# Kernel tuning notes

Measured on AMD Instinct MI355X. Metric: run time of the kernel, lower is better.

The kernel has to match this reference:

```python
import jax, jax.numpy as jnp
import numpy as np

B, N, K, H, W = 8, 16, 128, 64, 64
POS_RATE = 0.002  # fraction of positive heatmap pixels


def setup_inputs() -> dict:
    key = jax.random.key(0)
    k1, k2, k3 = jax.random.split(key, 3)
    # scores in (0.01, 0.99) so log(s) and log(1-s) are finite
    all_scores = jax.random.uniform(k1, (B, K, N), dtype=jnp.float32) * 0.98 + 0.01
    gt_heatmap = (jax.random.uniform(k2, (B, N, H, W)) < POS_RATE).astype(jnp.float32)
    # guarantee at least one positive pixel per heatmap (original errors on empty nonzero)
    gt_heatmap = gt_heatmap.at[:, :, 0, 0].set(1.0)
    keypoints_list = jax.random.uniform(k3, (B, K, 2), dtype=jnp.float32) * H
    return {"all_scores": all_scores, "gt_heatmap": gt_heatmap, "keypoints_list": keypoints_list}


def reference(all_scores, gt_heatmap, keypoints_list):
    Bs, Ns, Hs, Ws = gt_heatmap.shape
    # pixel coordinates in (row, col) order, matching torch nonzero() output
    hh, ww = jnp.meshgrid(jnp.arange(Hs, dtype=jnp.float32),
                          jnp.arange(Ws, dtype=jnp.float32), indexing='ij')
    coords = jnp.stack([hh.ravel(), ww.ravel()], axis=-1)  # [HW, 2]

    # distance from every candidate keypoint to every pixel: [B, K, HW]
    diff = keypoints_list[:, :, None, :] - coords[None, None, :, :]
    dist = jnp.sqrt(jnp.sum(diff * diff, axis=-1))

    mask = gt_heatmap.reshape(Bs, Ns, -1) > 0  # [B, N, HW]
    # min distance to any ground-truth pixel of heatmap n: [B, N, K]
    dmin = jnp.min(jnp.where(mask[:, :, None, :], dist[:, None, :, :], jnp.inf), axis=-1)

    scores = jnp.transpose(all_scores, (0, 2, 1))  # [B, N, K]
    pos = dmin < 1.0
    dsafe = jnp.where(pos, dmin, 0.0)  # avoid inf/overflow in unused branch
    pos_loss = jnp.sum(jnp.where(pos, 10000.0 / (1.0 + jnp.exp(dsafe)) * jnp.log(scores), 0.0))
    neg_loss = jnp.sum(jnp.where(pos, 0.0, jnp.log(1.0 - scores)))
    neg_count = jnp.sum(~pos)

    loss = -pos_loss - jnp.where(neg_count > 0,
                                 10000.0 / neg_count.astype(jnp.float32) * neg_loss,
                                 0.0)
    return loss
```

## Files before the change

### kernel.cpp

```cpp
#include <hip/hip_runtime.h>

#define BB 8
#define NN 16
#define KK 128
#define HH 64
#define WW 64
#define HWPX (HH * WW)

__global__ __launch_bounds__(256) void kp_loss_partials(
    const float* __restrict__ all_scores,
    const float* __restrict__ gt_heatmap,
    const float* __restrict__ keypoints,
    float* __restrict__ partials)
{
    __shared__ float sh_r[HWPX];
    __shared__ float sh_c[HWPX];
    __shared__ int   sh_count;
    __shared__ float red0[256], red1[256], red2[256];

    const int blk = blockIdx.x;
    const int b   = blk / NN;
    const int n   = blk % NN;
    const int tid = threadIdx.x;

    if (tid == 0) sh_count = 0;
    __syncthreads();

    const float* hm = gt_heatmap + (size_t)blk * HWPX;
    for (int i = tid; i < HWPX; i += 256) {
        if (hm[i] > 0.0f) {
            int slot = atomicAdd(&sh_count, 1);
            sh_r[slot] = (float)(i >> 6);
            sh_c[slot] = (float)(i & (WW - 1));
        }
    }
    __syncthreads();
    const int cnt = sh_count;

    float pos_c = 0.0f, neg_c = 0.0f, ncnt = 0.0f;
    if (tid < KK) {
        const int k = tid;
        const float kr = keypoints[((size_t)b * KK + k) * 2 + 0];
        const float kc = keypoints[((size_t)b * KK + k) * 2 + 1];
        float dmin2 = INFINITY;
        for (int m = 0; m < cnt; ++m) {
            const float dr = kr - sh_r[m];
            const float dc = kc - sh_c[m];
            dmin2 = fminf(dmin2, dr * dr + dc * dc);
        }
        const float score = all_scores[((size_t)b * KK + k) * NN + n];
        if (dmin2 < 1.0f) {
            const float dmin = sqrtf(dmin2);
            pos_c = 10000.0f / (1.0f + __expf(dmin)) * __logf(score);
        } else {
            neg_c = __logf(1.0f - score);
            ncnt  = 1.0f;
        }
    }

    red0[tid] = pos_c; red1[tid] = neg_c; red2[tid] = ncnt;
    __syncthreads();
    for (int s = 128; s > 0; s >>= 1) {
        if (tid < s) {
            red0[tid] += red0[tid + s];
            red1[tid] += red1[tid + s];
            red2[tid] += red2[tid + s];
        }
        __syncthreads();
    }
    if (tid == 0) {
        partials[blk * 3 + 0] = red0[0];
        partials[blk * 3 + 1] = red1[0];
        partials[blk * 3 + 2] = red2[0];
    }
}

__global__ __launch_bounds__(128) void kp_loss_finalize(
    const float* __restrict__ partials, float* __restrict__ out)
{
    __shared__ float red0[128], red1[128], red2[128];
    const int tid = threadIdx.x;
    red0[tid] = partials[tid * 3 + 0];
    red1[tid] = partials[tid * 3 + 1];
    red2[tid] = partials[tid * 3 + 2];
    __syncthreads();
    for (int s = 64; s > 0; s >>= 1) {
        if (tid < s) {
            red0[tid] += red0[tid + s];
            red1[tid] += red1[tid + s];
            red2[tid] += red2[tid + s];
        }
        __syncthreads();
    }
    if (tid == 0) {
        const float pos_sum = red0[0];
        const float neg_sum = red1[0];
        const float cnt     = red2[0];
        float loss = -pos_sum;
        if (cnt > 0.0f) loss -= (10000.0f / cnt) * neg_sum;
        out[0] = loss;
    }
}

extern "C" void kernel_launch(void* const* d_in, const int* in_sizes, int n_in,
                              void* d_out, int out_size, void* d_ws, size_t ws_size,
                              hipStream_t stream) {
    const float* all_scores = (const float*)d_in[0];
    const float* gt_heatmap = (const float*)d_in[1];
    const float* keypoints  = (const float*)d_in[2];
    float* out = (float*)d_out;
    float* partials = (float*)d_ws;

    kp_loss_partials<<<BB * NN, 256, 0, stream>>>(all_scores, gt_heatmap, keypoints, partials);
    kp_loss_finalize<<<1, 128, 0, stream>>>(partials, out);
}
```

Measured before the change: 12.24 us.

## Fuse partial and final reduction into one cooperative kernel with grid sync

Merges the two kernels into a single cooperative launch that uses a grid-wide sync before block 0 reduces the per-block partials, removing the second launch. Blocks shrink from 256 to 128 threads so every thread handles a keypoint, heatmap loads are vectorised to float4, and the shared-memory tree reductions become wavefront shuffle reductions. A cooperative launch and grid barrier have their own overhead, and the atomic slot ordering now differs.

```diff
diff --git a/kernel.cpp b/kernel.cpp
--- a/kernel.cpp
+++ b/kernel.cpp
@@ -1,4 +1,7 @@
 #include <hip/hip_runtime.h>
+#include <hip/hip_cooperative_groups.h>
+
+namespace cg = cooperative_groups;
 
 #define BB 8
 #define NN 16
@@ -7,98 +10,93 @@
 #define WW 64
 #define HWPX (HH * WW)
 
-__global__ __launch_bounds__(256) void kp_loss_partials(
+__global__ __launch_bounds__(128) void kp_loss_fused(
     const float* __restrict__ all_scores,
     const float* __restrict__ gt_heatmap,
     const float* __restrict__ keypoints,
-    float* __restrict__ partials)
+    float* __restrict__ partials,
+    float* __restrict__ out)
 {
     __shared__ float sh_r[HWPX];
     __shared__ float sh_c[HWPX];
     __shared__ int   sh_count;
-    __shared__ float red0[256], red1[256], red2[256];
+    __shared__ float wred[2][3];
 
-    const int blk = blockIdx.x;
-    const int b   = blk / NN;
-    const int n   = blk % NN;
-    const int tid = threadIdx.x;
+    const int blk  = blockIdx.x;
+    const int b    = blk >> 4;
+    const int n    = blk & (NN - 1);
+    const int tid  = threadIdx.x;
+    const int lane = tid & 63;
+    const int wid  = tid >> 6;
 
     if (tid == 0) sh_count = 0;
     __syncthreads();
 
-    const float* hm = gt_heatmap + (size_t)blk * HWPX;
-    for (int i = tid; i < HWPX; i += 256) {
-        if (hm[i] > 0.0f) {
-            int slot = atomicAdd(&sh_count, 1);
-            sh_r[slot] = (float)(i >> 6);
-            sh_c[slot] = (float)(i & (WW - 1));
-        }
+    const float4* hm = (const float4*)(gt_heatmap + (size_t)blk * HWPX);
+    for (int i = tid; i < HWPX / 4; i += 128) {
+        const float4 v = hm[i];
+        const int base = i << 2;
+        const float row = (float)(base >> 6);
+        const float col = (float)(base & (WW - 1));
+        if (v.x > 0.0f) { int s = atomicAdd(&sh_count, 1); sh_r[s] = row; sh_c[s] = col; }
+        if (v.y > 0.0f) { int s = atomicAdd(&sh_count, 1); sh_r[s] = row; sh_c[s] = col + 1.0f; }
+        if (v.z > 0.0f) { int s = atomicAdd(&sh_count, 1); sh_r[s] = row; sh_c[s] = col + 2.0f; }
+        if (v.w > 0.0f) { int s = atomicAdd(&sh_count, 1); sh_r[s] = row; sh_c[s] = col + 3.0f; }
     }
     __syncthreads();
     const int cnt = sh_count;
 
-    float pos_c = 0.0f, neg_c = 0.0f, ncnt = 0.0f;
-    if (tid < KK) {
-        const int k = tid;
-        const float kr = keypoints[((size_t)b * KK + k) * 2 + 0];
-        const float kc = keypoints[((size_t)b * KK + k) * 2 + 1];
-        float dmin2 = INFINITY;
-        for (int m = 0; m < cnt; ++m) {
-            const float dr = kr - sh_r[m];
-            const float dc = kc - sh_c[m];
-            dmin2 = fminf(dmin2, dr * dr + dc * dc);
-        }
-        const float score = all_scores[((size_t)b * KK + k) * NN + n];
-        if (dmin2 < 1.0f) {
-            const float dmin = sqrtf(dmin2);
-            pos_c = 10000.0f / (1.0f + __expf(dmin)) * __logf(score);
-        } else {
-            neg_c = __logf(1.0f - score);
-            ncnt  = 1.0f;
-        }
+    const float kr = keypoints[((size_t)b * KK + tid) * 2 + 0];
+    const float kc = keypoints[((size_t)b * KK + tid) * 2 + 1];
+    float dmin2 = INFINITY;
+    for (int m = 0; m < cnt; ++m) {
+        const float dr = kr - sh_r[m];
+        const float dc = kc - sh_c[m];
+        dmin2 = fminf(dmin2, dr * dr + dc * dc);
+    }
+    const float score = all_scores[((size_t)b * KK + tid) * NN + n];
+    float r0 = 0.0f, r1 = 0.0f, r2 = 0.0f;
+    if (dmin2 < 1.0f) {
+        r0 = 10000.0f / (1.0f + __expf(sqrtf(dmin2))) * __logf(score);
+    } else {
+        r1 = __logf(1.0f - score);
+        r2 = 1.0f;
     }
 
-    red0[tid] = pos_c; red1[tid] = neg_c; red2[tid] = ncnt;
+    for (int off = 32; off > 0; off >>= 1) {
+        r0 += __shfl_down(r0, off);
+        r1 += __shfl_down(r1, off);
+        r2 += __shfl_down(r2, off);
+    }
+    if (lane == 0) { wred[wid][0] = r0; wred[wid][1] = r1; wred[wid][2] = r2; }
     __syncthreads();
-    for (int s = 128; s > 0; s >>= 1) {
-        if (tid < s) {
-            red0[tid] += red0[tid + s];
-            red1[tid] += red1[tid + s];
-            red2[tid] += red2[tid + s];
+    if (tid == 0) {
+        partials[blk * 3 + 0] = wred[0][0] + wred[1][0];
+        partials[blk * 3 + 1] = wred[0][1] + wred[1][1];
+        partials[blk * 3 + 2] = wred[0][2] + wred[1][2];
+    }
+
+    cg::this_grid().sync();
+
+    if (blk == 0) {
+        float p0 = partials[tid * 3 + 0];
+        float p1 = partials[tid * 3 + 1];
+        float p2 = partials[tid * 3 + 2];
+        for (int off = 32; off > 0; off >>= 1) {
+            p0 += __shfl_down(p0, off);
+            p1 += __shfl_down(p1, off);
+            p2 += __shfl_down(p2, off);
         }
+        if (lane == 0) { wred[wid][0] = p0; wred[wid][1] = p1; wred[wid][2] = p2; }
         __syncthreads();
-    }
-    if (tid == 0) {
-        partials[blk * 3 + 0] = red0[0];
-        partials[blk * 3 + 1] = red1[0];
-        partials[blk * 3 + 2] = red2[0];
-    }
-}
-
-__global__ __launch_bounds__(128) void kp_loss_finalize(
-    const float* __restrict__ partials, float* __restrict__ out)
-{
-    __shared__ float red0[128], red1[128], red2[128];
-    const int tid = threadIdx.x;
-    red0[tid] = partials[tid * 3 + 0];
-    red1[tid] = partials[tid * 3 + 1];
-    red2[tid] = partials[tid * 3 + 2];
-    __syncthreads();
-    for (int s = 64; s > 0; s >>= 1) {
-        if (tid < s) {
-            red0[tid] += red0[tid + s];
-            red1[tid] += red1[tid + s];
-            red2[tid] += red2[tid + s];
+        if (tid == 0) {
+            const float pos_sum = wred[0][0] + wred[1][0];
+            const float neg_sum = wred[0][1] + wred[1][1];
+            const float cntf    = wred[0][2] + wred[1][2];
+            float loss = -pos_sum;
+            if (cntf > 0.0f) loss -= (10000.0f / cntf) * neg_sum;
+            out[0] = loss;
         }
-        __syncthreads();
-    }
-    if (tid == 0) {
-        const float pos_sum = red0[0];
-        const float neg_sum = red1[0];
-        const float cnt     = red2[0];
-        float loss = -pos_sum;
-        if (cnt > 0.0f) loss -= (10000.0f / cnt) * neg_sum;
-        out[0] = loss;
     }
 }
 
@@ -108,9 +106,11 @@
     const float* all_scores = (const float*)d_in[0];
     const float* gt_heatmap = (const float*)d_in[1];
     const float* keypoints  = (const float*)d_in[2];
-    float* out = (float*)d_out;
+    float* out      = (float*)d_out;
     float* partials = (float*)d_ws;
 
-    kp_loss_partials<<<BB * NN, 256, 0, stream>>>(all_scores, gt_heatmap, keypoints, partials);
-    kp_loss_finalize<<<1, 128, 0, stream>>>(partials, out);
+    void* args[] = { (void*)&all_scores, (void*)&gt_heatmap, (void*)&keypoints,
+                     (void*)&partials, (void*)&out };
+    hipLaunchCooperativeKernel((void*)kp_loss_fused, dim3(BB * NN), dim3(128),
+                               args, 0, stream);
 }
```

New measurement: 43.37 us. 3.54x slower.
